# Kernel optimization log

Measured on AMD Instinct MI355X. Metric: run time of the kernel, lower is better.

Reference implementation:

```python
import jax, jax.numpy as jnp
import numpy as np

DIM = 512
BATCH = 256
LOG_2PI = float(np.log(2.0 * np.pi))


def setup_inputs() -> dict:
    key = jax.random.key(0)
    k_x, k_mu, k_ld, k_lt, k_m = jax.random.split(key, 5)
    n_tril = DIM * (DIM - 1) // 2  # 130816
    x = jax.random.normal(k_x, (BATCH, DIM), dtype=jnp.float32)
    mu = jax.random.normal(k_mu, (DIM,), dtype=jnp.float32)
    log_diagonal = jax.random.normal(k_ld, (DIM,), dtype=jnp.float32)
    # scale strict-lower entries for reasonable conditioning of cov = A A^T
    lower_tri = jax.random.normal(k_lt, (n_tril,), dtype=jnp.float32) * 0.05
    mask = jax.random.randint(k_m, (BATCH, DIM), 0, 2) > 0
    return {"x": x, "mu": mu, "log_diagonal": log_diagonal,
            "lower_tri": lower_tri, "mask": mask}


def _build_cov(log_diagonal, lower_tri):
    D = log_diagonal.shape[0]
    ti, tj = np.tril_indices(D, -1)
    A = jnp.zeros((D, D), dtype=log_diagonal.dtype).at[ti, tj].set(lower_tri)
    A = A + jnp.diag(jnp.exp(log_diagonal))
    return A @ A.T  # SPD covariance [D, D]


def reference(x, mu, log_diagonal, lower_tri, mask):
    cov = _build_cov(log_diagonal, lower_tri)          # [D, D]
    m = mask.astype(x.dtype)                           # [B, D]
    D = cov.shape[0]
    # Block-diagonalized masked covariance: observed block = cov[m][:,m],
    # unobserved block = identity. Equivalent to per-sample submatrix gather.
    cov_m = (m[:, :, None] * m[:, None, :]) * cov[None] \
            + jnp.eye(D, dtype=x.dtype)[None] * (1.0 - m)[:, :, None]  # [B, D, D]
    L = jnp.linalg.cholesky(cov_m)                     # batched [B, D, D]
    r = (x - mu) * m                                   # masked residual [B, D]
    z = jax.scipy.linalg.solve_triangular(L, r[..., None], lower=True)[..., 0]
    quad = jnp.sum(z * z, axis=-1)                     # [B]
    # unobserved diag of L is 1 -> contributes 0 to logdet
    logdet = 2.0 * jnp.sum(jnp.log(jnp.diagonal(L, axis1=-2, axis2=-1)), axis=-1)
    d_obs = jnp.sum(m, axis=-1)
    return 0.5 * (quad + logdet + d_obs * LOG_2PI)     # neg log prob, [B]
```

## Files before the change

kernel.cpp:

```cpp
#include <hip/hip_runtime.h>
#include <hip/hip_bf16.h>

#define LOG_2PI 1.8378770664093453f
#define R0 256
#define GSTRIDE 512
#define TRI_FLOATS 33280
#define CSTR 68
#define NT 256
#define SMEM_FLOATS (TRI_FLOATS + 512 + 512 + 512 + 16 + 64*CSTR)
#define SMEM_BYTES (SMEM_FLOATS * 4)

__device__ __forceinline__ int tribase(int r) {
    int m = r & 3;
    return r * (r + 1) / 2 + 6 * (r >> 2) + ((m * (7 - m)) >> 1);
}

__global__ __launch_bounds__(256) void prep2(const float* __restrict__ logd,
                                             const float* __restrict__ lt,
                                             const float* __restrict__ x,
                                             const float* __restrict__ mu,
                                             const int* __restrict__ mask,
                                             float* __restrict__ A,
                                             int* __restrict__ obs_idx,
                                             int* __restrict__ n_obs,
                                             float* __restrict__ rc) {
    if (blockIdx.x < 1024) {
        int idx = blockIdx.x * 256 + threadIdx.x;
        int i = idx >> 9, j = idx & 511;
        float v;
        if (j < i)       v = lt[(i * (i - 1)) / 2 + j];
        else if (j == i) v = expf(logd[i]);
        else             v = 0.f;
        A[idx] = v;
    } else {
        __shared__ int wsum[4];
        int b = blockIdx.x - 1024, t = threadIdx.x;
        int i0 = 2 * t, i1 = 2 * t + 1;
        int m0 = (mask[b * 512 + i0] != 0) ? 1 : 0;
        int m1 = (mask[b * 512 + i1] != 0) ? 1 : 0;
        int local = m0 + m1;
        int v = local;
        int lane = t & 63, wv = t >> 6;
        #pragma unroll
        for (int off = 1; off < 64; off <<= 1) {
            int u = __shfl_up(v, off, 64);
            if (lane >= off) v += u;
        }
        if (lane == 63) wsum[wv] = v;
        __syncthreads();
        int woff = 0;
        for (int w = 0; w < wv; w++) woff += wsum[w];
        int excl = woff + v - local;
        if (m0) { obs_idx[b * 512 + excl] = i0; rc[b * 512 + excl] = x[b * 512 + i0] - mu[i0]; }
        if (m1) { int p = excl + m0; obs_idx[b * 512 + p] = i1; rc[b * 512 + p] = x[b * 512 + i1] - mu[i1]; }
        if (t == 0) n_obs[b] = wsum[0] + wsum[1] + wsum[2] + wsum[3];
    }
}

__global__ __launch_bounds__(256) void aat(const float* __restrict__ A,
                                           float* __restrict__ C) {
    __shared__ float Ash[32][33];
    __shared__ float Bsh[32][33];
    int tx = threadIdx.x & 31, ty = threadIdx.x >> 5;
    int bi = blockIdx.y, bj = blockIdx.x;
    float acc[4] = {0.f, 0.f, 0.f, 0.f};
    for (int k0 = 0; k0 < 512; k0 += 32) {
        #pragma unroll
        for (int q = 0; q < 4; q++) {
            int r = ty + q * 8;
            Ash[r][tx] = A[(bi * 32 + r) * 512 + k0 + tx];
            Bsh[r][tx] = A[(bj * 32 + r) * 512 + k0 + tx];
        }
        __syncthreads();
        for (int c = 0; c < 32; c++) {
            float bv = Bsh[tx][c];
            #pragma unroll
            for (int q = 0; q < 4; q++) acc[q] += Ash[ty + q * 8][c] * bv;
        }
        __syncthreads();
    }
    #pragma unroll
    for (int q = 0; q < 4; q++)
        C[(bi * 32 + ty + q * 8) * 512 + bj * 32 + tx] = acc[q];
}

template <typename RPF>
__device__ __forceinline__ void diag_block(RPF rptr, float* zsh, float* dinvAll,
                                           float& llog, int j0, int nb, int n, int tid) {
    if (tid < 32) {
        int l = tid;
        int r = j0 + l;
        float a[32];
        float z = 0.f;
        if (r < n) {
            const float4* src = (const float4*)(rptr(r) + j0);
            #pragma unroll
            for (int q = 0; q < 8; q++) {
                float4 t = src[q];
                a[4*q+0] = t.x; a[4*q+1] = t.y; a[4*q+2] = t.z; a[4*q+3] = t.w;
            }
            z = zsh[r];
        } else {
            #pragma unroll
            for (int q = 0; q < 32; q++) a[q] = 0.f;
        }
        float dv = 0.f;
        #pragma unroll
        for (int k = 0; k < 32; k++) {
            if (k < nb) {
                float akk = __shfl(a[k], k, 64);
                float rin = rsqrtf(akk);
                float lkk = akk * rin;
                if (l == k) { dv = rin; llog += __logf(lkk); }
                a[k] = (l == k) ? lkk : a[k] * rin;
                #pragma unroll
                for (int j = k + 1; j < 32; j++) {
                    float ajk = __shfl(a[k], j, 64);
                    a[j] -= a[k] * ajk;
                }
            }
        }
        #pragma unroll
        for (int k = 0; k < 32; k++) {
            if (k < nb) {
                if (l == k) z *= dv;
                float zk = __shfl(z, k, 64);
                if (l > k) z -= a[k] * zk;
            }
        }
        dinvAll[j0 + l] = dv;
        if (l < nb) {
            zsh[r] = z;
            float* dst = rptr(r) + j0;
            #pragma unroll
            for (int c = 0; c < 32; c++)
                if (c <= l) dst[c] = a[c];
        }
    }
}

__device__ __forceinline__ void syrk_macro32(float* T, int rbase0, int cbase0,
                                             int j0, int n0, int lane, bool diag) {
    int ty = lane >> 3, tx = lane & 7;
    int rbase = rbase0 + ty * 4, cbase = cbase0 + tx * 4;
    if (diag && cbase > rbase + 3) return;
    int ra[4], rb[4];
    #pragma unroll
    for (int a = 0; a < 4; a++) {
        ra[a] = tribase(min(rbase + a, n0 - 1)) + j0;
        rb[a] = tribase(min(cbase + a, n0 - 1)) + j0;
    }
    float acc[4][4];
    #pragma unroll
    for (int a = 0; a < 4; a++)
        #pragma unroll
        for (int c = 0; c < 4; c++) acc[a][c] = 0.f;
    #pragma unroll
    for (int q = 0; q < 8; q++) {
        float4 av[4], bv[4];
        #pragma unroll
        for (int a = 0; a < 4; a++) av[a] = *(const float4*)&T[ra[a] + 4 * q];
        #pragma unroll
        for (int c = 0; c < 4; c++) bv[c] = *(const float4*)&T[rb[c] + 4 * q];
        #pragma unroll
        for (int a = 0; a < 4; a++)
            #pragma unroll
            for (int c = 0; c < 4; c++)
                acc[a][c] += av[a].x*bv[c].x + av[a].y*bv[c].y +
                             av[a].z*bv[c].z + av[a].w*bv[c].w;
    }
    #pragma unroll
    for (int a = 0; a < 4; a++) {
        int r = rbase + a;
        if (r < n0) {
            float* trow = T + tribase(r);
            if (cbase + 3 <= r) {
                float4 v = *(const float4*)&trow[cbase];
                v.x -= acc[a][0]; v.y -= acc[a][1];
                v.z -= acc[a][2]; v.w -= acc[a][3];
                *(float4*)&trow[cbase] = v;
            } else {
                #pragma unroll
                for (int c = 0; c < 4; c++) {
                    int cl = cbase + c;
                    if (cl <= r) trow[cl] -= acc[a][c];
                }
            }
        }
    }
}

__global__ __launch_bounds__(NT) void chol_solve(
    const float* __restrict__ cov, const float* __restrict__ rc,
    const int* __restrict__ obs_idx, const int* __restrict__ n_obs,
    float* __restrict__ gtail_all, float* __restrict__ out) {

    extern __shared__ float smem[];
    float* T       = smem;
    float* zsh     = T + TRI_FLOATS;
    int*   oi      = (int*)(zsh + 512);
    float* dinvAll = (float*)(oi + 512);
    float* red     = dinvAll + 512;
    float* SBc     = red + 16;

    int b = blockIdx.x, tid = threadIdx.x;
    int lane = tid & 63, wv = tid >> 6;
    int n = n_obs[b]; if (n > 512) n = 512;
    float* gtail = gtail_all + (size_t)b * 256 * GSTRIDE;
    if (n == 0) { if (tid == 0) out[b] = 0.f; return; }

    for (int i = tid; i < n; i += NT) {
        oi[i] = obs_idx[b * 512 + i];
        zsh[i] = rc[b * 512 + i];
    }
    __syncthreads();

    int n0 = (n < R0) ? n : R0;
    int ntail = n - n0;

    for (int r = wv; r < n0; r += 4) {
        const float* crow = cov + (size_t)oi[r] * 512;
        float* dst = T + tribase(r);
        #pragma unroll 4
        for (int j = lane; j <= r; j += 64) dst[j] = crow[oi[j]];
    }
    for (int r = n0 + wv; r < n; r += 4) {
        const float* crow = cov + (size_t)oi[r] * 512;
        float* dst = gtail + (size_t)(r - n0) * GSTRIDE;
        #pragma unroll 4
        for (int j = lane; j < n0; j += 64) dst[j] = crow[oi[j]];
    }
    __syncthreads();

    float llog = 0.f;

    for (int j0 = 0; j0 < n0; j0 += 32) {
        int nb = min(32, n0 - j0);
        diag_block([&](int r) { return T + tribase(r); },
                   zsh, dinvAll, llog, j0, nb, n0, tid);
        __syncthreads();

        int mL = n0 - j0 - 32; if (mL < 0) mL = 0;
        int mtot = mL + ntail;
        if (mtot == 0) continue;

        {
            float dvv[32];
            #pragma unroll
            for (int q = 0; q < 8; q++) {
                float4 t4 = *(const float4*)&dinvAll[j0 + 4 * q];
                dvv[4*q+0] = t4.x; dvv[4*q+1] = t4.y;
                dvv[4*q+2] = t4.z; dvv[4*q+3] = t4.w;
            }
            for (int idx = tid; idx < mtot; idx += NT) {
                int r; float* prow;
                if (idx < mL) { r = j0 + 32 + idx; prow = T + tribase(r) + j0; }
                else          { r = n0 + (idx - mL);
                                prow = gtail + (size_t)(idx - mL) * GSTRIDE + j0; }
                float p[32];
                #pragma unroll
                for (int q = 0; q < 8; q++) {
                    float4 t = *(const float4*)&prow[4 * q];
                    p[4*q+0] = t.x; p[4*q+1] = t.y; p[4*q+2] = t.z; p[4*q+3] = t.w;
                }
                #pragma unroll
                for (int j = 0; j < 32; j++) {
                    const float* dj = T + tribase(j0 + j) + j0;
                    float s0 = 0.f, s1 = 0.f, s2 = 0.f, s3 = 0.f;
                    int jf = j >> 2;
                    for (int q2 = 0; q2 < jf; q2++) {
                        float4 t = *(const float4*)&dj[q2 * 4];
                        s0 += p[q2*4+0]*t.x; s1 += p[q2*4+1]*t.y;
                        s2 += p[q2*4+2]*t.z; s3 += p[q2*4+3]*t.w;
                    }
                    float acc = p[j] - ((s0 + s1) + (s2 + s3));
                    for (int c = jf * 4; c < j; c++) acc -= p[c] * dj[c];
                    p[j] = acc * dvv[j];
                }
                float zu = 0.f;
                #pragma unroll
                for (int q = 0; q < 8; q++) {
                    *(float4*)&prow[4 * q] = make_float4(p[4*q], p[4*q+1], p[4*q+2], p[4*q+3]);
                    float4 zz = *(const float4*)&zsh[j0 + 4 * q];
                    zu += p[4*q]*zz.x + p[4*q+1]*zz.y + p[4*q+2]*zz.z + p[4*q+3]*zz.w;
                }
                zsh[r] -= zu;
            }
        }
        __syncthreads();

        if (mL > 0) {
            int nMac = (mL + 31) >> 5;
            int pairs = nMac * (nMac + 1) / 2;
            for (int e = wv; e < pairs; e += 4) {
                int MI = 0;
                while ((MI + 1) * (MI + 2) / 2 <= e) MI++;
                int MJ = e - MI * (MI + 1) / 2;
                syrk_macro32(T, j0 + 32 + MI * 32, j0 + 32 + MJ * 32,
                             j0, n0, lane, MI == MJ);
            }
        }

        if (ntail > 0 && mL > 0) {
            int nRM = (ntail + 31) >> 5;
            int nCM = mL >> 5;
            int tot = nRM * nCM;
            int ty = lane >> 3, tx = lane & 7;
            for (int e = wv; e < tot; e += 4) {
                int MI = e / nCM, MJ = e % nCM;
                int r0 = MI * 32 + ty * 4;
                int c0 = j0 + 32 + MJ * 32 + tx * 4;
                int rb[4], tcb[4];
                #pragma unroll
                for (int a = 0; a < 4; a++) {
                    rb[a] = min(r0 + a, ntail - 1);
                    tcb[a] = tribase(min(c0 + a, n0 - 1)) + j0;
                }
                float acc[4][4];
                #pragma unroll
                for (int a = 0; a < 4; a++)
                    #pragma unroll
                    for (int c = 0; c < 4; c++) acc[a][c] = 0.f;
                #pragma unroll
                for (int q = 0; q < 8; q++) {
                    float4 av[4], bv[4];
                    #pragma unroll
                    for (int a = 0; a < 4; a++)
                        av[a] = *(const float4*)&gtail[(size_t)rb[a] * GSTRIDE + j0 + 4 * q];
                    #pragma unroll
                    for (int c = 0; c < 4; c++)
                        bv[c] = *(const float4*)&T[tcb[c] + 4 * q];
                    #pragma unroll
                    for (int a = 0; a < 4; a++)
                        #pragma unroll
                        for (int c = 0; c < 4; c++)
                            acc[a][c] += av[a].x*bv[c].x + av[a].y*bv[c].y +
                                         av[a].z*bv[c].z + av[a].w*bv[c].w;
                }
                #pragma unroll
                for (int a = 0; a < 4; a++) {
                    int r = r0 + a;
                    if (r < ntail) {
                        float* grow = gtail + (size_t)r * GSTRIDE;
                        float4 g4 = *(const float4*)&grow[c0];
                        g4.x -= acc[a][0]; g4.y -= acc[a][1];
                        g4.z -= acc[a][2]; g4.w -= acc[a][3];
                        *(float4*)&grow[c0] = g4;
                    }
                }
            }
        }
        __syncthreads();
    }

    for (int gs2 = R0; gs2 < n; gs2 += 64) {
        int t1 = min(64, n - gs2);
        int g1 = gs2 - R0;

        for (int cp = R0; cp < gs2; cp += 32) {
            if (tid < t1) {
                int r = gs2 + tid;
                float* row = gtail + (size_t)(r - R0) * GSTRIDE;
                const float* crow = cov + (size_t)oi[r] * 512;
                float zacc = 0.f;
                for (int j = 0; j < 32; j++) {
                    int jj = cp + j;
                    const float* Lrow = gtail + (size_t)(jj - R0) * GSTRIDE;
                    float s0 = 0.f, s1 = 0.f, s2 = 0.f, s3 = 0.f;
                    int jv = jj >> 2;
                    for (int c4 = 0; c4 < jv; c4++) {
                        float4 a4 = *(const float4*)&row[c4 * 4];
                        float4 b4 = *(const float4*)&Lrow[c4 * 4];
                        s0 += a4.x*b4.x; s1 += a4.y*b4.y;
                        s2 += a4.z*b4.z; s3 += a4.w*b4.w;
                    }
                    float acc = crow[oi[jj]] - ((s0 + s1) + (s2 + s3));
                    for (int c = jv * 4; c < jj; c++) acc -= row[c] * Lrow[c];
                    float wv2 = acc * dinvAll[jj];
                    row[jj] = wv2;
                    zacc += wv2 * zsh[jj];
                }
                zsh[r] -= zacc;
            }
            __syncthreads();
        }

        {
            int npair = t1 * (t1 + 1) / 2;
            for (int e = tid; e < npair; e += NT) {
                int ti = (int)((sqrtf(8.f * (float)e + 1.f) - 1.f) * 0.5f);
                while ((ti + 1) * (ti + 2) / 2 <= e) ti++;
                while (ti * (ti + 1) / 2 > e) ti--;
                int tj = e - ti * (ti + 1) / 2;
                const float* wa = gtail + (size_t)(g1 + ti) * GSTRIDE;
                const float* wb = gtail + (size_t)(g1 + tj) * GSTRIDE;
                float s0 = 0.f, s1 = 0.f, s2 = 0.f, s3 = 0.f;
                for (int k = 0; k < gs2; k += 4) {
                    float4 a4 = *(const float4*)&wa[k];
                    float4 b4 = *(const float4*)&wb[k];
                    s0 += a4.x*b4.x; s1 += a4.y*b4.y;
                    s2 += a4.z*b4.z; s3 += a4.w*b4.w;
                }
                SBc[ti * CSTR + tj] = cov[(size_t)oi[gs2 + ti] * 512 + oi[gs2 + tj]]
                                      - ((s0 + s1) + (s2 + s3));
            }
        }
        __syncthreads();

        auto crptr = [&](int r) { return SBc + (r - gs2) * CSTR - gs2; };
        diag_block(crptr, zsh, dinvAll, llog, gs2, min(32, t1), n, tid);
        __syncthreads();
        if (t1 > 32) {
            int t2 = t1 - 32;
            if (tid < t2) {
                int r = gs2 + 32 + tid;
                float* prow = SBc + (32 + tid) * CSTR;
                float p[32];
                #pragma unroll
                for (int q = 0; q < 8; q++) {
                    float4 t = *(const float4*)&prow[4 * q];
                    p[4*q+0] = t.x; p[4*q+1] = t.y; p[4*q+2] = t.z; p[4*q+3] = t.w;
                }
                #pragma unroll
                for (int j = 0; j < 32; j++) {
                    const float* dj = SBc + j * CSTR;
                    float s0 = 0.f, s1 = 0.f, s2 = 0.f, s3 = 0.f;
                    int jf = j >> 2;
                    for (int q2 = 0; q2 < jf; q2++) {
                        float4 t = *(const float4*)&dj[q2 * 4];
                        s0 += p[q2*4+0]*t.x; s1 += p[q2*4+1]*t.y;
                        s2 += p[q2*4+2]*t.z; s3 += p[q2*4+3]*t.w;
                    }
                    float acc = p[j] - ((s0 + s1) + (s2 + s3));
                    for (int c = jf * 4; c < j; c++) acc -= p[c] * dj[c];
                    p[j] = acc * dinvAll[gs2 + j];
                }
                float zu = 0.f;
                #pragma unroll
                for (int q = 0; q < 8; q++) {
                    *(float4*)&prow[4 * q] = make_float4(p[4*q], p[4*q+1], p[4*q+2], p[4*q+3]);
                    float4 zz = *(const float4*)&zsh[gs2 + 4 * q];
                    zu += p[4*q]*zz.x + p[4*q+1]*zz.y + p[4*q+2]*zz.z + p[4*q+3]*zz.w;
                }
                zsh[r] -= zu;
            }
            __syncthreads();
            int np2 = t2 * (t2 + 1) / 2;
            for (int e = tid; e < np2; e += NT) {
                int ti = (int)((sqrtf(8.f * (float)e + 1.f) - 1.f) * 0.5f);
                while ((ti + 1) * (ti + 2) / 2 <= e) ti++;
                while (ti * (ti + 1) / 2 > e) ti--;
                int tj = e - ti * (ti + 1) / 2;
                const float* wa = SBc + (32 + ti) * CSTR;
                const float* wb = SBc + (32 + tj) * CSTR;
                float s0 = 0.f, s1 = 0.f, s2 = 0.f, s3 = 0.f;
                #pragma unroll
                for (int q = 0; q < 8; q++) {
                    float4 a4 = *(const float4*)&wa[4 * q];
                    float4 b4 = *(const float4*)&wb[4 * q];
                    s0 += a4.x*b4.x; s1 += a4.y*b4.y;
                    s2 += a4.z*b4.z; s3 += a4.w*b4.w;
                }
                SBc[(32 + ti) * CSTR + 32 + tj] -= (s0 + s1) + (s2 + s3);
            }
            __syncthreads();
            diag_block(crptr, zsh, dinvAll, llog, gs2 + 32, min(32, t2), n, tid);
            __syncthreads();
        }
        if (gs2 + 64 < n) {
            for (int e = tid; e < t1 * 64; e += NT) {
                int i = e >> 6, j = e & 63;
                if (j <= i && i < t1)
                    gtail[(size_t)(g1 + i) * GSTRIDE + gs2 + j] = SBc[i * CSTR + j];
            }
            __syncthreads();
        }
    }

    float q = 0.f;
    for (int ii = tid; ii < n; ii += NT) { float zv = zsh[ii]; q += zv * zv; }
    #pragma unroll
    for (int off = 32; off; off >>= 1) {
        q    += __shfl_down(q, off, 64);
        llog += __shfl_down(llog, off, 64);
    }
    if (lane == 0) { red[wv] = q; red[8 + wv] = llog; }
    __syncthreads();
    if (tid == 0) {
        float qt = red[0] + red[1] + red[2] + red[3];
        float ls = red[8] + red[9] + red[10] + red[11];
        out[b] = 0.5f * (qt + 2.f * ls + (float)n * LOG_2PI);
    }
}

extern "C" void kernel_launch(void* const* d_in, const int* in_sizes, int n_in,
                              void* d_out, int out_size, void* d_ws, size_t ws_size,
                              hipStream_t stream) {
    const float* x    = (const float*)d_in[0];
    const float* mu   = (const float*)d_in[1];
    const float* logd = (const float*)d_in[2];
    const float* lt   = (const float*)d_in[3];
    const int*   mask = (const int*)d_in[4];
    float* out = (float*)d_out;

    char* ws = (char*)d_ws;
    float* cov     = (float*)(ws);
    float* A       = (float*)(ws + 1048576);
    int*   n_obs   = (int*)  (ws + 2097152);
    int*   obs_idx = (int*)  (ws + 2098176);
    float* rc      = (float*)(ws + 2622464);
    float* gtail   = (float*)(ws + 3146752);

    (void)hipFuncSetAttribute((const void*)chol_solve,
                              hipFuncAttributeMaxDynamicSharedMemorySize,
                              SMEM_BYTES);

    prep2<<<1280, 256, 0, stream>>>(logd, lt, x, mu, mask, A, obs_idx, n_obs, rc);
    dim3 g(16, 16);
    aat<<<g, 256, 0, stream>>>(A, cov);
    chol_solve<<<256, NT, SMEM_BYTES, stream>>>(cov, rc, obs_idx, n_obs, gtail, out);
}
```

Baseline: 398.9 us.

## Fuse A*A^T covariance GEMM into chol_solve with grid-wide atomic barrier

Drops the separate aat kernel launch. Each of the 256 chol_solve blocks now computes one 32x32 tile of cov = A A^T, then all blocks wait on a global atomic counter (reset by prep2) before the Cholesky phase starts. This saves one launch and its gap, but it depends on all 256 blocks being resident at the same time to avoid deadlock, and it adds spin-wait latency.

```diff
diff --git a/kernel.cpp b/kernel.cpp
--- a/kernel.cpp
+++ b/kernel.cpp
@@ -23,7 +23,9 @@
                                              float* __restrict__ A,
                                              int* __restrict__ obs_idx,
                                              int* __restrict__ n_obs,
-                                             float* __restrict__ rc) {
+                                             float* __restrict__ rc,
+                                             int* __restrict__ cnt) {
+    if (blockIdx.x == 0 && threadIdx.x == 0) *cnt = 0;
     if (blockIdx.x < 1024) {
         int idx = blockIdx.x * 256 + threadIdx.x;
         int i = idx >> 9, j = idx & 511;
@@ -57,33 +59,6 @@
     }
 }
 
-__global__ __launch_bounds__(256) void aat(const float* __restrict__ A,
-                                           float* __restrict__ C) {
-    __shared__ float Ash[32][33];
-    __shared__ float Bsh[32][33];
-    int tx = threadIdx.x & 31, ty = threadIdx.x >> 5;
-    int bi = blockIdx.y, bj = blockIdx.x;
-    float acc[4] = {0.f, 0.f, 0.f, 0.f};
-    for (int k0 = 0; k0 < 512; k0 += 32) {
-        #pragma unroll
-        for (int q = 0; q < 4; q++) {
-            int r = ty + q * 8;
-            Ash[r][tx] = A[(bi * 32 + r) * 512 + k0 + tx];
-            Bsh[r][tx] = A[(bj * 32 + r) * 512 + k0 + tx];
-        }
-        __syncthreads();
-        for (int c = 0; c < 32; c++) {
-            float bv = Bsh[tx][c];
-            #pragma unroll
-            for (int q = 0; q < 4; q++) acc[q] += Ash[ty + q * 8][c] * bv;
-        }
-        __syncthreads();
-    }
-    #pragma unroll
-    for (int q = 0; q < 4; q++)
-        C[(bi * 32 + ty + q * 8) * 512 + bj * 32 + tx] = acc[q];
-}
-
 template <typename RPF>
 __device__ __forceinline__ void diag_block(RPF rptr, float* zsh, float* dinvAll,
                                            float& llog, int j0, int nb, int n, int tid) {
@@ -191,11 +166,55 @@
 }
 
 __global__ __launch_bounds__(NT) void chol_solve(
-    const float* __restrict__ cov, const float* __restrict__ rc,
-    const int* __restrict__ obs_idx, const int* __restrict__ n_obs,
-    float* __restrict__ gtail_all, float* __restrict__ out) {
+    const float* __restrict__ A, float* __restrict__ cov,
+    const float* __restrict__ rc, const int* __restrict__ obs_idx,
+    const int* __restrict__ n_obs, float* __restrict__ gtail_all,
+    int* __restrict__ cnt, float* __restrict__ out) {
 
     extern __shared__ float smem[];
+    int b = blockIdx.x, tid = threadIdx.x;
+    int lane = tid & 63, wv = tid >> 6;
+
+    {
+        float* Ash = smem;
+        float* Bsh = smem + 1056;
+        int tx = tid & 31, ty = tid >> 5;
+        int bi = b >> 4, bj = b & 15;
+        float acc[4] = {0.f, 0.f, 0.f, 0.f};
+        for (int k0 = 0; k0 < 512; k0 += 32) {
+            #pragma unroll
+            for (int q = 0; q < 4; q++) {
+                int r = ty + q * 8;
+                Ash[r * 33 + tx] = A[(bi * 32 + r) * 512 + k0 + tx];
+                Bsh[r * 33 + tx] = A[(bj * 32 + r) * 512 + k0 + tx];
+            }
+            __syncthreads();
+            for (int c = 0; c < 32; c++) {
+                float bv = Bsh[tx * 33 + c];
+                #pragma unroll
+                for (int q = 0; q < 4; q++) acc[q] += Ash[(ty + q * 8) * 33 + c] * bv;
+            }
+            __syncthreads();
+        }
+        #pragma unroll
+        for (int q = 0; q < 4; q++)
+            cov[(size_t)(bi * 32 + ty + q * 8) * 512 + bj * 32 + tx] = acc[q];
+    }
+
+    __syncthreads();
+    if (tid == 0) {
+        __threadfence();
+        __hip_atomic_fetch_add(cnt, 1, __ATOMIC_RELEASE, __HIP_MEMORY_SCOPE_AGENT);
+        long spin = 0;
+        while (__hip_atomic_load(cnt, __ATOMIC_ACQUIRE, __HIP_MEMORY_SCOPE_AGENT) < 256
+               && spin < 2000000000L) {
+            __builtin_amdgcn_s_sleep(8);
+            spin++;
+        }
+        __threadfence();
+    }
+    __syncthreads();
+
     float* T       = smem;
     float* zsh     = T + TRI_FLOATS;
     int*   oi      = (int*)(zsh + 512);
@@ -203,8 +222,6 @@
     float* red     = dinvAll + 512;
     float* SBc     = red + 16;
 
-    int b = blockIdx.x, tid = threadIdx.x;
-    int lane = tid & 63, wv = tid >> 6;
     int n = n_obs[b]; if (n > 512) n = 512;
     float* gtail = gtail_all + (size_t)b * 256 * GSTRIDE;
     if (n == 0) { if (tid == 0) out[b] = 0.f; return; }
@@ -509,14 +526,13 @@
     int*   n_obs   = (int*)  (ws + 2097152);
     int*   obs_idx = (int*)  (ws + 2098176);
     float* rc      = (float*)(ws + 2622464);
-    float* gtail   = (float*)(ws + 3146752);
+    int*   cnt     = (int*)  (ws + 3146752);
+    float* gtail   = (float*)(ws + 3147776);
 
     (void)hipFuncSetAttribute((const void*)chol_solve,
                               hipFuncAttributeMaxDynamicSharedMemorySize,
                               SMEM_BYTES);
 
-    prep2<<<1280, 256, 0, stream>>>(logd, lt, x, mu, mask, A, obs_idx, n_obs, rc);
-    dim3 g(16, 16);
-    aat<<<g, 256, 0, stream>>>(A, cov);
-    chol_solve<<<256, NT, SMEM_BYTES, stream>>>(cov, rc, obs_idx, n_obs, gtail, out);
+    prep2<<<1280, 256, 0, stream>>>(logd, lt, x, mu, mask, A, obs_idx, n_obs, rc, cnt);
+    chol_solve<<<256, NT, SMEM_BYTES, stream>>>(A, cov, rc, obs_idx, n_obs, gtail, cnt, out);
 }
```

Result: slower. 425.9 us (+6.8%).
